# Optimization experiments

Measured on AMD Instinct MI355X. Metric: run time of the kernel, lower is better.

The kernel has to match this reference:

```python
import jax, jax.numpy as jnp
import numpy as np

NUM_CLASSES = 21
THRESH = 0.5
NEG_POS = 3
VAR0, VAR1 = 0.1, 0.2


def point_form(boxes):
    # center form (cx,cy,w,h) -> corner form (x1,y1,x2,y2)
    return jnp.concatenate([boxes[:, :2] - boxes[:, 2:] / 2,
                            boxes[:, :2] + boxes[:, 2:] / 2], axis=1)


def jaccard(a, b):
    # a: [N,4] corner form, b: [P,4] corner form -> IoU [N,P]
    lt = jnp.maximum(a[:, None, :2], b[None, :, :2])
    rb = jnp.minimum(a[:, None, 2:], b[None, :, 2:])
    wh = jnp.clip(rb - lt, 0.0)
    inter = wh[..., 0] * wh[..., 1]
    area_a = (a[:, 2] - a[:, 0]) * (a[:, 3] - a[:, 1])
    area_b = (b[:, 2] - b[:, 0]) * (b[:, 3] - b[:, 1])
    return inter / (area_a[:, None] + area_b[None, :] - inter)


def match_one(truths, labels, priors):
    # truths: [N,4] corner form, labels: [N] int, priors: [P,4] center form
    ov = jaccard(truths, point_form(priors))            # [N,P]
    best_prior_idx = jnp.argmax(ov, axis=1)             # [N] best prior per truth
    best_truth_ov = jnp.max(ov, axis=0)                 # [P]
    best_truth_idx = jnp.argmax(ov, axis=0)             # [P]
    # ensure each truth keeps its best prior
    best_truth_ov = best_truth_ov.at[best_prior_idx].set(2.0)
    best_truth_idx = best_truth_idx.at[best_prior_idx].set(
        jnp.arange(truths.shape[0], dtype=best_truth_idx.dtype))
    matches = truths[best_truth_idx]                    # [P,4]
    conf = labels[best_truth_idx] + 1                   # [P]
    conf = jnp.where(best_truth_ov < THRESH, 0, conf)
    # encode
    g_cxcy = ((matches[:, :2] + matches[:, 2:]) / 2 - priors[:, :2]) / (VAR0 * priors[:, 2:])
    g_wh = jnp.log((matches[:, 2:] - matches[:, :2]) / priors[:, 2:]) / VAR1
    return jnp.concatenate([g_cxcy, g_wh], axis=1), conf


def setup_inputs() -> dict:
    key = jax.random.key(0)
    k1, k2, k3, k4, k5, k6, k7 = jax.random.split(key, 7)
    B, P, C, N = 64, 24564, NUM_CLASSES, 16
    loc_data = jax.random.normal(k1, (B, P, 4), dtype=jnp.float32)
    conf_data = jax.random.normal(k2, (B, P, C), dtype=jnp.float32)
    # priors: valid center-form boxes
    ctr = 0.05 + 0.9 * jax.random.uniform(k3, (P, 2), dtype=jnp.float32)
    pwh = 0.05 + 0.25 * jax.random.uniform(k4, (P, 2), dtype=jnp.float32)
    priors = jnp.concatenate([ctr, pwh], axis=1)
    # truths: valid corner-form boxes
    xy1 = 0.7 * jax.random.uniform(k5, (B, N, 2), dtype=jnp.float32)
    twh = 0.05 + 0.2 * jax.random.uniform(k6, (B, N, 2), dtype=jnp.float32)
    truths = jnp.concatenate([xy1, xy1 + twh], axis=2)
    labels = jax.random.randint(k7, (B, N), 0, 20, dtype=jnp.int32)
    return {"loc_data": loc_data, "conf_data": conf_data, "priors": priors,
            "truths": truths, "labels": labels}


def reference(loc_data, conf_data, priors, truths, labels):
    B, P, C = conf_data.shape
    loc_t, conf_t = jax.vmap(lambda t, l: match_one(t, l, priors))(truths, labels)
    pos = conf_t > 0                                     # [B,P]

    # localization smooth-L1, summed over positives
    diff = loc_data - loc_t
    ad = jnp.abs(diff)
    sl1 = jnp.where(ad < 1.0, 0.5 * diff * diff, ad - 0.5)
    loss_l = jnp.sum(sl1 * pos[..., None].astype(loc_data.dtype))

    # per-prior CE = logsumexp - logit at matched class
    lse = jax.nn.logsumexp(conf_data, axis=2)            # [B,P]
    gathered = jnp.take_along_axis(conf_data, conf_t[..., None].astype(jnp.int32), axis=2)[..., 0]
    loss_c_all = lse - gathered

    # hard-negative mining via double argsort rank (pos zeroed first)
    loss_c_mine = jnp.where(pos, 0.0, loss_c_all)
    idx_rank = jnp.argsort(jnp.argsort(-loss_c_mine, axis=1), axis=1)
    num_pos = jnp.sum(pos, axis=1, keepdims=True)        # [B,1]
    num_neg = jnp.minimum(NEG_POS * num_pos, P - 1)
    neg = idx_rank < num_neg

    mask = pos | neg
    loss_c = jnp.sum(jnp.where(mask, loss_c_all, 0.0))

    n = jnp.sum(num_pos).astype(loc_data.dtype)
    return loss_l / n, loss_c / n
```

## Files before the change

kernel.cpp:

```cpp
#include <hip/hip_runtime.h>
#include <cstdint>
#include <cstddef>

#define B_ 64
#define P_ 24564
#define C_ 21
#define N_ 16
#define NPL_ 96
#define THRESH_ 0.5f


__device__ inline unsigned long long shfl_down_u64(unsigned long long v, int off) {
    unsigned lo = (unsigned)v, hi = (unsigned)(v >> 32);
    lo = __shfl_down(lo, off);
    hi = __shfl_down(hi, off);
    return ((unsigned long long)hi << 32) | lo;
}

__device__ inline void async_copy16(const float* g, float* l) {
    __builtin_amdgcn_global_load_lds(
        (const __attribute__((address_space(1))) void*)g,
        (__attribute__((address_space(3))) void*)l, 16, 0, 0);
}

__device__ inline float sl1_encode(float4 ld, float4 pr,
                                   float tx1, float ty1, float tx2, float ty2) {
    float gcx = ((tx1 + tx2) * 0.5f - pr.x) / (0.1f * pr.z);
    float gcy = ((ty1 + ty2) * 0.5f - pr.y) / (0.1f * pr.w);
    float gw  = __logf((tx2 - tx1) / pr.z) / 0.2f;
    float gh  = __logf((ty2 - ty1) / pr.w) / 0.2f;
    float g[4] = {gcx, gcy, gw, gh};
    float l[4] = {ld.x, ld.y, ld.z, ld.w};
    float s = 0.0f;
#pragma unroll
    for (int i = 0; i < 4; i++) {
        float d = l[i] - g[i];
        float ad = fabsf(d);
        s += (ad < 1.0f) ? 0.5f * d * d : ad - 0.5f;
    }
    return s;
}


__global__ __launch_bounds__(256, 4) void
kF_fused(const float* __restrict__ loc,
         const float* __restrict__ conf,
         const float* __restrict__ priors,
         const float* __restrict__ truths,
         const int* __restrict__ labels,
         float* __restrict__ mine,
         float* __restrict__ part_ll,
         float* __restrict__ part_pce,
         int* __restrict__ part_np,
         unsigned long long* __restrict__ part_key) {
    int b = blockIdx.y, bx = blockIdx.x, t = threadIdx.x;
    int wid = t >> 6, lane = t & 63;
    __shared__ float scf[256 * C_];
    __shared__ unsigned skey[N_ * 256];
    __shared__ int lb[N_];
    __shared__ float sll[4], spc[4];
    __shared__ int snp[4];

    int base_p = bx * 256;
    int nvalid = min(256, P_ - base_p);
    int maxf4 = (nvalid * C_) >> 2;
    const float* gtile = conf + ((size_t)b * P_ + base_p) * C_;

    for (int k = wid; k < 21; k += 4) {
        int f4 = k * 64 + lane;
        int s4 = (f4 < maxf4) ? f4 : (maxf4 - 1);
        async_copy16(gtile + (size_t)s4 * 4, scf + k * 256);
    }
    if (t < N_) lb[t] = labels[b * N_ + t];

    int p0 = base_p + t;
    bool valid = t < nvalid;
    float4 pr = ((const float4*)priors)[valid ? p0 : base_p];
    float px1 = pr.x - pr.z * 0.5f, py1 = pr.y - pr.w * 0.5f;
    float px2 = pr.x + pr.z * 0.5f, py2 = pr.y + pr.w * 0.5f;
    float ap = (px2 - px1) * (py2 - py1);

    float best = -1.0f;
    int bn = 0;
#pragma unroll
    for (int n = 0; n < N_; n++) {
        float4 tb = ((const float4*)truths)[b * N_ + n];
        float at = (tb.z - tb.x) * (tb.w - tb.y);
        float lx = fmaxf(tb.x, px1), ly = fmaxf(tb.y, py1);
        float rx = fminf(tb.z, px2), ry = fminf(tb.w, py2);
        float w = fmaxf(rx - lx, 0.0f), h = fmaxf(ry - ly, 0.0f);
        float inter = w * h;
        float iou = inter / (at + ap - inter);
        if (iou > best) { best = iou; bn = n; }
        skey[n * 256 + t] = valid ? __float_as_uint(iou) : 0u;
    }
    int pos = (valid && best >= THRESH_) ? 1 : 0;

    __syncthreads();

#pragma unroll
    for (int i = 0; i < 4; i++) {
        int n = wid + 4 * i;
        unsigned long long bk = 0ull;
#pragma unroll
        for (int q = 0; q < 4; q++) {
            int tt = lane + 64 * q;
            unsigned k32 = skey[n * 256 + tt];
            unsigned long long v = ((unsigned long long)k32 << 32) |
                                   (unsigned)~(unsigned)tt;
            bk = (v > bk) ? v : bk;
        }
        for (int off = 32; off; off >>= 1) {
            unsigned long long o = shfl_down_u64(bk, off);
            bk = (o > bk) ? o : bk;
        }
        if (lane == 0) {
            int twin = (int)~(unsigned)(bk & 0xFFFFFFFFull);
            unsigned k32 = (unsigned)(bk >> 32);
            int pwin = base_p + twin;
            part_key[(size_t)(b * NPL_ + bx) * N_ + n] =
                ((unsigned long long)k32 << 32) | (unsigned)~(unsigned)pwin;
        }
    }

    float ll = 0.0f, pce = 0.0f;
    int np = 0;
    if (valid) {
        int cls = pos ? (lb[bn] + 1) : 0;
        float ssum = 0.0f;
#pragma unroll
        for (int i = 0; i < 21; i++) ssum += __expf(scf[t * 21 + i]);
        float g = scf[t * 21 + cls];
        float lca = fmaxf(__logf(ssum) - g, 0.0f);

        mine[(size_t)b * P_ + p0] = pos ? 0.0f : lca;

        if (pos) {
            np = 1;
            pce = lca;
            float4 ld = ((const float4*)loc)[(size_t)b * P_ + p0];
            float4 tb = ((const float4*)truths)[b * N_ + bn];
            ll = sl1_encode(ld, pr, tb.x, tb.y, tb.z, tb.w);
        }
    }

    for (int off = 32; off; off >>= 1) {
        ll += __shfl_down(ll, off);
        pce += __shfl_down(pce, off);
        np += __shfl_down(np, off);
    }
    if (lane == 0) { sll[wid] = ll; spc[wid] = pce; snp[wid] = np; }
    __syncthreads();
    if (t == 0) {
        float a = 0.0f, cc = 0.0f;
        int q = 0;
        for (int i = 0; i < 4; i++) { a += sll[i]; cc += spc[i]; q += snp[i]; }
        part_ll[b * NPL_ + bx] = a;
        part_pce[b * NPL_ + bx] = cc;
        part_np[b * NPL_ + bx] = q;
    }
}

__global__ __launch_bounds__(1024) void
kB_batch(const float* __restrict__ loc,
         const float* __restrict__ conf,
         const float* __restrict__ priors,
         const float* __restrict__ truths,
         const int* __restrict__ labels,
         const float* __restrict__ mine,
         const float* __restrict__ part_ll,
         const float* __restrict__ part_pce,
         const int* __restrict__ part_np,
         const unsigned long long* __restrict__ part_key,
         double* __restrict__ bll,
         double* __restrict__ bpc,
         int* __restrict__ bnp) {
    int b = blockIdx.x, t = threadIdx.x, wid = t >> 6, lane = t & 63;
    __shared__ float tr[N_ * 4];
    __shared__ int lb[N_];
    __shared__ unsigned long long skmax[N_];
    __shared__ int sp[N_];
    __shared__ float sdll, sdpce, sll_s, spc_s;
    __shared__ int sdnp, snp_s;
    __shared__ int scnt[16];
    __shared__ unsigned sT;
    __shared__ float wsum[16];
    __shared__ int wcgt[16];

    if (t < N_ * 4) tr[t] = truths[b * N_ * 4 + t];
    if (t < N_) { lb[t] = labels[b * N_ + t]; skmax[t] = 0ull; }
    if (t == 0) { sdll = 0.f; sdpce = 0.f; sdnp = 0; sll_s = 0.f; spc_s = 0.f; snp_s = 0; }
    __syncthreads();
    if (t < 256) {
        int n = t & 15, j = t >> 4;
        unsigned long long bk = 0ull;
        for (int i = j; i < NPL_; i += 16) {
            unsigned long long k = part_key[(size_t)(b * NPL_ + i) * N_ + n];
            bk = (k > bk) ? k : bk;
        }
        atomicMax(&skmax[n], bk);
    }
    if (t < NPL_) {
        atomicAdd(&sll_s, part_ll[b * NPL_ + t]);
        atomicAdd(&spc_s, part_pce[b * NPL_ + t]);
        atomicAdd(&snp_s, part_np[b * NPL_ + t]);
    }
    __syncthreads();
    if (t < N_) sp[t] = (int)~(unsigned)(skmax[t] & 0xFFFFFFFFull);
    __syncthreads();
    if (t < N_) {
        int p = sp[t];
        bool last = true;
        for (int n = t + 1; n < N_; n++) if (sp[n] == p) last = false;
        if (last) {
            int nf = t;
            float4 pr = ((const float4*)priors)[p];
            float px1 = pr.x - pr.z * 0.5f, py1 = pr.y - pr.w * 0.5f;
            float px2 = pr.x + pr.z * 0.5f, py2 = pr.y + pr.w * 0.5f;
            float ap = (px2 - px1) * (py2 - py1);
            float best = -1.0f;
            int bti = 0;
            for (int n = 0; n < N_; n++) {
                float tx1 = tr[n * 4], ty1 = tr[n * 4 + 1];
                float tx2 = tr[n * 4 + 2], ty2 = tr[n * 4 + 3];
                float at = (tx2 - tx1) * (ty2 - ty1);
                float lx = fmaxf(tx1, px1), ly = fmaxf(ty1, py1);
                float rx = fminf(tx2, px2), ry = fminf(ty2, py2);
                float w = fmaxf(rx - lx, 0.0f), h = fmaxf(ry - ly, 0.0f);
                float inter = w * h;
                float iou = inter / (at + ap - inter);
                if (iou > best) { best = iou; bti = n; }
            }
            int pos_old = (best >= THRESH_) ? 1 : 0;
            const float* cp = conf + ((size_t)b * P_ + p) * C_;
            float x[C_];
            float ssum = 0.0f;
            for (int j = 0; j < C_; j++) { x[j] = cp[j]; ssum += __expf(x[j]); }
            float lse = __logf(ssum);
            float4 ld = ((const float4*)loc)[(size_t)b * P_ + p];
            float dll = sl1_encode(ld, pr, tr[nf * 4], tr[nf * 4 + 1],
                                   tr[nf * 4 + 2], tr[nf * 4 + 3]);
            float dpce = lse - x[lb[nf] + 1];
            int dnp = 1 - pos_old;
            if (pos_old) {
                dll -= sl1_encode(ld, pr, tr[bti * 4], tr[bti * 4 + 1],
                                  tr[bti * 4 + 2], tr[bti * 4 + 3]);
                dpce -= lse - x[lb[bti] + 1];
            }
            atomicAdd(&sdll, dll);
            atomicAdd(&sdpce, dpce);
            atomicAdd(&sdnp, dnp);
        }
    }

    unsigned omask = 0;
#pragma unroll
    for (int n = 0; n < N_; n++) {
        int p = sp[n];
        if ((p & 1023) == t) omask |= 1u << (p >> 10);
    }
    const float* v = mine + (size_t)b * P_;
    int nel = (t < (P_ - 23 * 1024)) ? 24 : 23;
    float xv[24];
#pragma unroll
    for (int i = 0; i < 24; i++) {
        float x = 0.0f;
        if (i < nel) x = v[t + (i << 10)];
        if ((omask >> i) & 1) x = 0.0f;
        xv[i] = x;
    }
    __syncthreads();
    int np = snp_s + sdnp;
    int k = np * 3;
    if (k > P_ - 1) k = P_ - 1;

    unsigned T = 0u;
    for (int bpos = 30; bpos >= 0; bpos--) {
        unsigned cand = T | (1u << bpos);
        int c = 0;
#pragma unroll
        for (int i = 0; i < 24; i++)
            if (__float_as_uint(xv[i]) >= cand) c++;
        for (int off = 32; off; off >>= 1) c += __shfl_down(c, off);
        if (lane == 0) scnt[wid] = c;
        __syncthreads();
        if (t == 0) {
            int tot = 0;
            for (int i = 0; i < 16; i++) tot += scnt[i];
            sT = (tot >= k) ? cand : T;
        }
        __syncthreads();
        T = sT;
    }

    float psum = 0.0f;
    int cgt = 0;
#pragma unroll
    for (int i = 0; i < 24; i++) {
        if (__float_as_uint(xv[i]) > T) { psum += xv[i]; cgt++; }
    }
    for (int off = 32; off; off >>= 1) {
        psum += __shfl_down(psum, off);
        cgt += __shfl_down(cgt, off);
    }
    if (lane == 0) { wsum[wid] = psum; wcgt[wid] = cgt; }
    __syncthreads();
    if (t == 0) {
        float s2 = 0.0f;
        int cg = 0;
        for (int i = 0; i < 16; i++) { s2 += wsum[i]; cg += wcgt[i]; }
        int skrem = k - cg;
        double tot = (double)s2 + (double)skrem * (double)__uint_as_float(T);
        bll[b] = (double)(sll_s + sdll);
        bpc[b] = (double)(spc_s + sdpce) + tot;
        bnp[b] = np;
    }
}

__global__ void kC_final(const double* __restrict__ bll,
                         const double* __restrict__ bpc,
                         const int* __restrict__ bnp,
                         float* __restrict__ out) {
    int t = threadIdx.x;
    double a = bll[t], c = bpc[t];
    int n = bnp[t];
    for (int off = 32; off; off >>= 1) {
        a += __shfl_down(a, off);
        c += __shfl_down(c, off);
        n += __shfl_down(n, off);
    }
    if (t == 0) {
        double dn = (double)n;
        out[0] = (float)(a / dn);
        out[1] = (float)(c / dn);
    }
}


extern "C" void kernel_launch(void* const* d_in, const int* in_sizes, int n_in,
                              void* d_out, int out_size, void* d_ws, size_t ws_size,
                              hipStream_t stream) {
    const float* loc    = (const float*)d_in[0];
    const float* conf   = (const float*)d_in[1];
    const float* priors = (const float*)d_in[2];
    const float* truths = (const float*)d_in[3];
    const int*   labels = (const int*)d_in[4];
    float* out = (float*)d_out;

    char* ws = (char*)d_ws;
    unsigned long long* part_key = (unsigned long long*)(ws);
    float*  part_ll  = (float*)(ws + 786432);
    float*  part_pce = (float*)(ws + 811008);
    int*    part_np  = (int*)(ws + 835584);
    double* bll      = (double*)(ws + 860160);
    double* bpc      = (double*)(ws + 860672);
    int*    bnp      = (int*)(ws + 861184);
    float*  mine     = (float*)(ws + 1048576);

    hipLaunchKernelGGL(kF_fused, dim3(NPL_, B_), dim3(256), 0, stream,
                       loc, conf, priors, truths, labels,
                       mine, part_ll, part_pce, part_np, part_key);
    hipLaunchKernelGGL(kB_batch, dim3(B_), dim3(1024), 0, stream,
                       loc, conf, priors, truths, labels, mine,
                       part_ll, part_pce, part_np, part_key, bll, bpc, bnp);
    hipLaunchKernelGGL(kC_final, dim3(1), dim3(64), 0, stream, bll, bpc, bnp, out);
}
```

Measured before the change: 259.3 us.

## Replace shared-memory argmax with wave shuffles and halve radix-select barriers

In the fused match kernel, each wave now computes the per-truth max IoU with shuffle-xor and a ballot-based first-lane tie break, and writes one key per wave. This replaces the 16x256 shared IoU table and the 64-bit shuffle reduction, which frees shared memory, and the occupancy hint rises from 4 to 6 blocks. In the mining kernel, partial sums are reduced with wave shuffles before the atomics, and each radix-select bit step accumulates into its own shared counter slot, removing one barrier and the serial thread-0 sum per step. Conf logits are re-read from global memory instead of being kept in a register array.

```diff
diff --git a/kernel.cpp b/kernel.cpp
--- a/kernel.cpp
+++ b/kernel.cpp
@@ -9,13 +9,6 @@
 #define NPL_ 96
 #define THRESH_ 0.5f
 
-
-__device__ inline unsigned long long shfl_down_u64(unsigned long long v, int off) {
-    unsigned lo = (unsigned)v, hi = (unsigned)(v >> 32);
-    lo = __shfl_down(lo, off);
-    hi = __shfl_down(hi, off);
-    return ((unsigned long long)hi << 32) | lo;
-}
 
 __device__ inline void async_copy16(const float* g, float* l) {
     __builtin_amdgcn_global_load_lds(
@@ -42,7 +35,7 @@
 }
 
 
-__global__ __launch_bounds__(256, 4) void
+__global__ __launch_bounds__(256, 6) void
 kF_fused(const float* __restrict__ loc,
          const float* __restrict__ conf,
          const float* __restrict__ priors,
@@ -56,7 +49,7 @@
     int b = blockIdx.y, bx = blockIdx.x, t = threadIdx.x;
     int wid = t >> 6, lane = t & 63;
     __shared__ float scf[256 * C_];
-    __shared__ unsigned skey[N_ * 256];
+    __shared__ unsigned long long swk[N_ * 4];
     __shared__ int lb[N_];
     __shared__ float sll[4], spc[4];
     __shared__ int snp[4];
@@ -92,35 +85,32 @@
         float inter = w * h;
         float iou = inter / (at + ap - inter);
         if (iou > best) { best = iou; bn = n; }
-        skey[n * 256 + t] = valid ? __float_as_uint(iou) : 0u;
+
+        unsigned k32 = valid ? __float_as_uint(iou) : 0u;
+        unsigned m = k32;
+#pragma unroll
+        for (int off = 32; off; off >>= 1) {
+            unsigned o = __shfl_xor(m, off);
+            m = (o > m) ? o : m;
+        }
+        unsigned long long msk = __ballot(k32 == m);
+        int wl = (int)__ffsll(msk) - 1;
+        if (lane == 0)
+            swk[n * 4 + wid] = ((unsigned long long)m << 32) |
+                               (unsigned)~(unsigned)(base_p + (wid << 6) + wl);
     }
     int pos = (valid && best >= THRESH_) ? 1 : 0;
 
     __syncthreads();
 
-#pragma unroll
-    for (int i = 0; i < 4; i++) {
-        int n = wid + 4 * i;
-        unsigned long long bk = 0ull;
-#pragma unroll
-        for (int q = 0; q < 4; q++) {
-            int tt = lane + 64 * q;
-            unsigned k32 = skey[n * 256 + tt];
-            unsigned long long v = ((unsigned long long)k32 << 32) |
-                                   (unsigned)~(unsigned)tt;
-            bk = (v > bk) ? v : bk;
-        }
-        for (int off = 32; off; off >>= 1) {
-            unsigned long long o = shfl_down_u64(bk, off);
+    if (t < N_) {
+        unsigned long long bk = swk[t * 4];
+#pragma unroll
+        for (int i = 1; i < 4; i++) {
+            unsigned long long o = swk[t * 4 + i];
             bk = (o > bk) ? o : bk;
         }
-        if (lane == 0) {
-            int twin = (int)~(unsigned)(bk & 0xFFFFFFFFull);
-            unsigned k32 = (unsigned)(bk >> 32);
-            int pwin = base_p + twin;
-            part_key[(size_t)(b * NPL_ + bx) * N_ + n] =
-                ((unsigned long long)k32 << 32) | (unsigned)~(unsigned)pwin;
-        }
+        part_key[(size_t)(b * NPL_ + bx) * N_ + t] = bk;
     }
 
     float ll = 0.0f, pce = 0.0f;
@@ -182,13 +172,13 @@
     __shared__ int sp[N_];
     __shared__ float sdll, sdpce, sll_s, spc_s;
     __shared__ int sdnp, snp_s;
-    __shared__ int scnt[16];
-    __shared__ unsigned sT;
+    __shared__ int scnt2[31];
     __shared__ float wsum[16];
     __shared__ int wcgt[16];
 
     if (t < N_ * 4) tr[t] = truths[b * N_ * 4 + t];
     if (t < N_) { lb[t] = labels[b * N_ + t]; skmax[t] = 0ull; }
+    if (t < 31) scnt2[t] = 0;
     if (t == 0) { sdll = 0.f; sdpce = 0.f; sdnp = 0; sll_s = 0.f; spc_s = 0.f; snp_s = 0; }
     __syncthreads();
     if (t < 256) {
@@ -200,10 +190,24 @@
         }
         atomicMax(&skmax[n], bk);
     }
-    if (t < NPL_) {
-        atomicAdd(&sll_s, part_ll[b * NPL_ + t]);
-        atomicAdd(&spc_s, part_pce[b * NPL_ + t]);
-        atomicAdd(&snp_s, part_np[b * NPL_ + t]);
+    if (t < 128) {
+        float a = 0.f, c2 = 0.f;
+        int q = 0;
+        if (t < NPL_) {
+            a = part_ll[b * NPL_ + t];
+            c2 = part_pce[b * NPL_ + t];
+            q = part_np[b * NPL_ + t];
+        }
+        for (int off = 32; off; off >>= 1) {
+            a += __shfl_down(a, off);
+            c2 += __shfl_down(c2, off);
+            q += __shfl_down(q, off);
+        }
+        if (lane == 0) {
+            atomicAdd(&sll_s, a);
+            atomicAdd(&spc_s, c2);
+            atomicAdd(&snp_s, q);
+        }
     }
     __syncthreads();
     if (t < N_) sp[t] = (int)~(unsigned)(skmax[t] & 0xFFFFFFFFull);
@@ -233,19 +237,18 @@
             }
             int pos_old = (best >= THRESH_) ? 1 : 0;
             const float* cp = conf + ((size_t)b * P_ + p) * C_;
-            float x[C_];
             float ssum = 0.0f;
-            for (int j = 0; j < C_; j++) { x[j] = cp[j]; ssum += __expf(x[j]); }
+            for (int j = 0; j < C_; j++) ssum += __expf(cp[j]);
             float lse = __logf(ssum);
             float4 ld = ((const float4*)loc)[(size_t)b * P_ + p];
             float dll = sl1_encode(ld, pr, tr[nf * 4], tr[nf * 4 + 1],
                                    tr[nf * 4 + 2], tr[nf * 4 + 3]);
-            float dpce = lse - x[lb[nf] + 1];
+            float dpce = lse - cp[lb[nf] + 1];
             int dnp = 1 - pos_old;
             if (pos_old) {
                 dll -= sl1_encode(ld, pr, tr[bti * 4], tr[bti * 4 + 1],
                                   tr[bti * 4 + 2], tr[bti * 4 + 3]);
-                dpce -= lse - x[lb[bti] + 1];
+                dpce -= lse - cp[lb[bti] + 1];
             }
             atomicAdd(&sdll, dll);
             atomicAdd(&sdpce, dpce);
@@ -282,15 +285,10 @@
         for (int i = 0; i < 24; i++)
             if (__float_as_uint(xv[i]) >= cand) c++;
         for (int off = 32; off; off >>= 1) c += __shfl_down(c, off);
-        if (lane == 0) scnt[wid] = c;
+        if (lane == 0) atomicAdd(&scnt2[30 - bpos], c);
         __syncthreads();
-        if (t == 0) {
-            int tot = 0;
-            for (int i = 0; i < 16; i++) tot += scnt[i];
-            sT = (tot >= k) ? cand : T;
-        }
-        __syncthreads();
-        T = sT;
+        int tot = scnt2[30 - bpos];
+        T = (tot >= k) ? cand : T;
     }
 
     float psum = 0.0f;
```

Result: slower. 266.4 us (+2.7%).
